# Performance work log

Measured on AMD Instinct MI355X. Metric: run time of the kernel, lower is better.

## Reference

```python
import jax, jax.numpy as jnp
import numpy as np

# cell: per-step concat([x_t, h, cost_t]) -> i2h (Linear to H), i2o (Linear to 1), no bias, no nonlinearity.

P = 16      # prod(kernel) = 4*4
H = 512     # hidden_length
D = P + H + 1  # input_shape = 529


def setup_inputs() -> dict:
    key = jax.random.key(0)
    k1, k2, k3, k4, k5 = jax.random.split(key, 5)
    B, T = 256, 2048
    x = jax.random.normal(k1, (B, T, 4, 4), dtype=jnp.float32)
    hidden = jax.random.normal(k2, (B, H), dtype=jnp.float32)
    cost = jax.random.uniform(k3, (B, T), dtype=jnp.float32)
    # Linear weights (torch convention: [out_features, in_features], bias=False)
    Wo = jax.random.normal(k4, (1, D), dtype=jnp.float32) / np.sqrt(D)
    Wh = jax.random.normal(k5, (H, D), dtype=jnp.float32) / np.sqrt(D)
    return {"x": x, "hidden": hidden, "cost": cost, "Wo": Wo, "Wh": Wh}


def reference(x, hidden, cost, Wo, Wh):
    B, T = x.shape[0], x.shape[1]
    xf = x.reshape(B, T, -1)            # [B, T, P] (flatten(2, -1))
    xs = jnp.swapaxes(xf, 0, 1)         # [T, B, P] for scan over time
    cs = cost.T                         # [T, B]

    def step(h, inp):
        xt, ct = inp                    # xt: [B,P], ct: [B]
        inter = jnp.concatenate([xt, h, ct[:, None]], axis=-1)  # [B, D]
        h_new = inter @ Wh.T            # i2h -> [B, H]
        o = (inter @ Wo.T)[:, 0]        # i2o -> [B], squeeze(-1)
        return h_new, o

    h_final, outs = jax.lax.scan(step, hidden, (xs, cs))
    return outs.T, h_final              # ([B, T], [B, H])
```

## Files before the change

### kernel.cpp

```cpp
#include <hip/hip_runtime.h>


typedef __attribute__((ext_vector_type(8))) _Float16 half8;
typedef __attribute__((ext_vector_type(4))) float f32x4;
typedef unsigned short u16;

#define KTOT 2176
#define NBIG 640

__device__ __forceinline__ u16 f2h(float f) {
  union { _Float16 h; u16 u; } v; v.h = (_Float16)f; return v.u;
}
__device__ __forceinline__ float h2f(u16 u) {
  union { u16 u; _Float16 h; } v; v.u = u; return (float)v.h;
}

typedef const __attribute__((address_space(1))) void* as1cv;
typedef __attribute__((address_space(3))) void* as3v;
__device__ __forceinline__ void gload16(const u16* g, u16* l) {
  __builtin_amdgcn_global_load_lds((as1cv)g, (as3v)l, 16, 0, 0);
}

__device__ __forceinline__ void wave_gemm_acc(const u16* __restrict__ A, int lda,
                                              const u16* __restrict__ Bt, int nstr,
                                              int kc0, int kcN, int lane,
                                              f32x4 (&acc)[4][4]) {
  const int q = lane >> 4, l15 = lane & 15;
  const u16* aP = A + (size_t)l15*lda + (size_t)kc0*32 + q*8;
  const u16* bP = Bt + ((size_t)kc0*nstr + l15)*32 + q*8;
  half8 a[4], b[4];
  #pragma unroll
  for (int rt = 0; rt < 4; ++rt) a[rt] = *(const half8*)(aP + (size_t)(rt*16)*lda);
  #pragma unroll
  for (int ct = 0; ct < 4; ++ct) b[ct] = *(const half8*)(bP + ct*512);
  for (int kc = kc0; kc < kcN; ++kc) {
    const u16* aN = aP + 32;
    const u16* bN = bP + (size_t)nstr*32;
    half8 an[4], bn[4];
    #pragma unroll
    for (int rt = 0; rt < 4; ++rt) an[rt] = *(const half8*)(aN + (size_t)(rt*16)*lda);
    #pragma unroll
    for (int ct = 0; ct < 4; ++ct) bn[ct] = *(const half8*)(bN + ct*512);
    #pragma unroll
    for (int rt = 0; rt < 4; ++rt)
      #pragma unroll
      for (int ct = 0; ct < 4; ++ct)
        acc[rt][ct] = __builtin_amdgcn_mfma_f32_16x16x32_f16(a[rt], b[ct], acc[rt][ct], 0,0,0);
    #pragma unroll
    for (int rt = 0; rt < 4; ++rt) a[rt] = an[rt];
    #pragma unroll
    for (int ct = 0; ct < 4; ++ct) b[ct] = bn[ct];
    aP = aN; bP = bN;
  }
}

__device__ __forceinline__ void wave_gemm(const u16* __restrict__ A, int lda,
                                          const u16* __restrict__ Bt, int nstr,
                                          int kc0, int kcN, int lane,
                                          f32x4 (&acc)[4][4]) {
  #pragma unroll
  for (int rt = 0; rt < 4; ++rt)
    #pragma unroll
    for (int ct = 0; ct < 4; ++ct) { f32x4 z = {0.f,0.f,0.f,0.f}; acc[rt][ct] = z; }
  wave_gemm_acc(A, lda, Bt, nstr, kc0, kcN, lane, acc);
}

__device__ __forceinline__ bool ksplit_reduce(f32x4 (&acc)[4][4], float* red,
                                              int wid, int lane) {
  if (wid > 0) {
    float* dst = red + (wid - 1) * 4096;
    #pragma unroll
    for (int rt = 0; rt < 4; ++rt)
      #pragma unroll
      for (int ct = 0; ct < 4; ++ct)
        *(f32x4*)(dst + ((rt*4 + ct)*64 + lane)*4) = acc[rt][ct];
  }
  __syncthreads();
  if (wid > 0) return false;
  #pragma unroll
  for (int w = 0; w < 3; ++w)
    #pragma unroll
    for (int rt = 0; rt < 4; ++rt)
      #pragma unroll
      for (int ct = 0; ct < 4; ++ct)
        acc[rt][ct] += *(const f32x4*)(red + w*4096 + ((rt*4 + ct)*64 + lane)*4);
  return true;
}

__device__ __forceinline__ void square_tile(const u16* __restrict__ Mp_in,
                                            const u16* __restrict__ Mt_in,
                                            u16* __restrict__ Mp_out,
                                            u16* __restrict__ Mt_out,
                                            int bx, float* red, int tid) {
  const int wid = tid >> 6, lane = tid & 63, q = lane >> 4, l15 = lane & 15;
  int row0 = (bx >> 3) * 64, c0 = (bx & 7) * 64;
  f32x4 acc[4][4];
  wave_gemm(Mp_in + (size_t)row0*512, 512, Mt_in + (size_t)c0*32, 512,
            wid*4, wid*4 + 4, lane, acc);
  if (!ksplit_reduce(acc, red, wid, lane)) return;
  #pragma unroll
  for (int rt = 0; rt < 4; ++rt)
    for (int ct = 0; ct < 4; ++ct)
      for (int r = 0; r < 4; ++r) {
        int row = row0 + rt*16 + q*4 + r, col = c0 + ct*16 + l15;
        u16 v = f2h(acc[rt][ct][r]);
        Mp_out[row*512 + col] = v;
        Mt_out[(row>>5)*16384 + col*32 + (row&31)] = v;
      }
}

__global__ __launch_bounds__(256) void prep_kernel(
    const float* __restrict__ Wh, const float* __restrict__ Wo,
    const float* __restrict__ hidden,
    u16* __restrict__ Mp0, u16* __restrict__ Mt0,
    u16* __restrict__ Sr, float* __restrict__ G,
    float* __restrict__ wod, u16* __restrict__ Hf, u16* __restrict__ Qs) {
  int idx = blockIdx.x * 256 + threadIdx.x;
  if (idx < 262144) {
    int k = idx >> 9, n = idx & 511;
    u16 v = f2h(Wh[n*529 + 16 + k]);
    Mp0[k*512 + n] = v;
    Mt0[(k>>5)*16384 + n*32 + (k&31)] = v;
    return;
  }
  idx -= 262144;
  if (idx < 8704) {
    int q = idx >> 9, n = idx & 511;
    u16 v = f2h(Wh[n*529 + (q < 16 ? q : 528)]);
    Sr[idx] = v;
    Qs[idx] = v;
    return;
  }
  idx -= 8704;
  if (idx < 512) { G[idx*128 + 0] = Wo[16 + idx]; return; }
  idx -= 512;
  if (idx < 17) { wod[idx] = Wo[idx < 16 ? idx : 528]; return; }
  idx -= 17;
  if (idx < 131072) Hf[idx] = f2h(hidden[idx]);
}

__global__ __launch_bounds__(256) void level_kernel(
    const u16* __restrict__ Mp_in, const u16* __restrict__ Mt_in,
    u16* __restrict__ Mp_out, u16* __restrict__ Mt_out,
    u16* __restrict__ Qs, float* __restrict__ G,
    const float* __restrict__ x, const float* __restrict__ cost,
    u16* __restrict__ A, int l) {
  __shared__ float red[12288];
  const int m = 1 << l;
  const int nq8 = (((17*m + 63) >> 6)) * 8;
  const int tid = threadIdx.x, bx = blockIdx.x;
  const int wid = tid >> 6, lane = tid & 63, q = lane >> 4, l15 = lane & 15;

  if (bx < 64) {
    square_tile(Mp_in, Mt_in, Mp_out, Mt_out, bx, red, tid);
    return;
  }
  if (bx < 64 + nq8) {
    int bq = bx - 64;
    int row0 = (bq >> 3) * 64, c0 = (bq & 7) * 64;
    f32x4 acc[4][4];
    wave_gemm(Qs + (size_t)row0*512, 512, Mt_in + (size_t)c0*32, 512,
              wid*4, wid*4 + 4, lane, acc);
    if (!ksplit_reduce(acc, red, wid, lane)) return;
    int lim = 17*m;
    #pragma unroll
    for (int rt = 0; rt < 4; ++rt)
      for (int ct = 0; ct < 4; ++ct)
        for (int r = 0; r < 4; ++r) {
          int rowIn = row0 + rt*16 + q*4 + r, col = c0 + ct*16 + l15;
          if (rowIn < lim) Qs[(size_t)(lim + rowIn)*512 + col] = f2h(acc[rt][ct][r]);
        }
    return;
  }
  if (bx < 64 + nq8 + 32) {
    int n0 = (bx - 64 - nq8) * 16;
    for (int idx = tid; idx < 16*m; idx += 256) {
      int c = idx & (m - 1), n = n0 + (idx >> l);
      const u16* mrow = Mp_in + n*512;
      float s0 = 0.f, s1 = 0.f, s2 = 0.f, s3 = 0.f;
      for (int k = 0; k < 512; k += 4) {
        s0 += h2f(mrow[k])   * G[k*128 + c];
        s1 += h2f(mrow[k+1]) * G[(k+1)*128 + c];
        s2 += h2f(mrow[k+2]) * G[(k+2)*128 + c];
        s3 += h2f(mrow[k+3]) * G[(k+3)*128 + c];
      }
      G[n*128 + m + c] = (s0 + s1) + (s2 + s3);
    }
    return;
  }
  int abx = bx - (64 + nq8 + 32);
  int r = (l*293 + abx)*2 + (tid >> 7);
  if (r >= 4096) return;
  int s = tid & 127;
  int i = r >> 8, b = r & 255, t = i*128 + s;
  const float* xp = x + ((size_t)b*2048 + t)*16;
  u16* ap = A + (size_t)r*KTOT + s*17;
  #pragma unroll
  for (int p = 0; p < 16; p += 4) {
    float4 v = *(const float4*)(xp + p);
    ap[p] = f2h(v.x); ap[p+1] = f2h(v.y); ap[p+2] = f2h(v.z); ap[p+3] = f2h(v.w);
  }
  ap[16] = f2h(cost[(size_t)b*2048 + t]);
}

__global__ void cbar_kernel(const u16* __restrict__ Sr, const float* __restrict__ G,
                            float* __restrict__ Cb) {
  int qq = blockIdx.x, lam = threadIdx.x;
  float s0 = 0.f, s1 = 0.f, s2 = 0.f, s3 = 0.f;
  for (int k = 0; k < 512; k += 4) {
    s0 += h2f(Sr[qq*512 + k])   * G[k*128 + lam];
    s1 += h2f(Sr[qq*512 + k+1]) * G[(k+1)*128 + lam];
    s2 += h2f(Sr[qq*512 + k+2]) * G[(k+2)*128 + lam];
    s3 += h2f(Sr[qq*512 + k+3]) * G[(k+3)*128 + lam];
  }
  Cb[qq*128 + lam] = (s0 + s1) + (s2 + s3);
}

__global__ void bbuild_kernel(const u16* __restrict__ Qs, const float* __restrict__ Cb,
                              const float* __restrict__ wod, const float* __restrict__ G,
                              u16* __restrict__ Bt, u16* __restrict__ Gt) {
  int idx = blockIdx.x * 256 + threadIdx.x;
  if (idx < KTOT * NBIG) {
    int krow = idx / NBIG, n = idx - krow * NBIG;
    int kc = krow >> 5, kk = krow & 31;
    int s = krow / 17, qq = krow - s * 17;
    u16 v;
    if (n < 512) {
      v = Qs[(size_t)((127 - s)*17 + qq)*512 + n];
    } else {
      int j = n - 512;
      if (s < j)       v = f2h(Cb[qq*128 + (j - 1 - s)]);
      else if (s == j) v = f2h(wod[qq]);
      else             v = 0;
    }
    Bt[(size_t)kc*(NBIG*32) + n*32 + kk] = v;
    return;
  }
  idx -= KTOT * NBIG;
  if (idx < 512*128) {
    int k = idx >> 7, j = idx & 127;
    Gt[(k>>5)*4096 + j*32 + (k&31)] = f2h(G[k*128 + j]);
  }
}

__global__ __launch_bounds__(256) void biggemm_kernel(const u16* __restrict__ A,
                                                      const u16* __restrict__ Bt,
                                                      u16* __restrict__ V0,
                                                      float* __restrict__ out,
                                                      const u16* __restrict__ Mp7,
                                                      const u16* __restrict__ Mt7,
                                                      u16* __restrict__ Mp8,
                                                      u16* __restrict__ Mt8) {
  __shared__ __align__(16) char smem[49152];
  const int bx = blockIdx.x, tid = threadIdx.x;
  if (bx >= 160) {
    float* red = (float*)smem;
    square_tile(Mp7, Mt7, Mp8, Mt8, bx - 160, red, tid);
    return;
  }
  u16* sA = (u16*)smem;
  u16* sB = (u16*)(smem + 16384);
  const int rowg = bx & 31, colg = bx >> 5;
  const int row0 = rowg * 128, c0 = colg * 128;
  const int wid = tid >> 6, lane = tid & 63;
  const int q = lane >> 4, l15 = lane & 15;
  const int wr = wid >> 1, wc = wid & 1;
  const int r4 = tid >> 2, ch = tid & 3;

  const u16* gA0 = A + (size_t)(row0 + r4) * KTOT + ch * 8;
  const u16* gB0 = Bt + (size_t)(c0 + r4) * 32 + ch * 8;
  const int lofs = r4 * 32 + ch * 8;

  f32x4 acc[4][4];
  #pragma unroll
  for (int rt = 0; rt < 4; ++rt)
    #pragma unroll
    for (int ct = 0; ct < 4; ++ct) { f32x4 z = {0.f,0.f,0.f,0.f}; acc[rt][ct] = z; }

  gload16(gA0,                     sA + lofs);
  gload16(gA0 + (size_t)64*KTOT,   sA + 2048 + lofs);
  gload16(gB0,                     sB + lofs);
  gload16(gB0 + 64*32,             sB + 2048 + lofs);
  __syncthreads();

  int cur = 0;
  for (int s = 0; s < 68; ++s) {
    if (s + 1 < 68) {
      const u16* ga = gA0 + (s + 1) * 32;
      const u16* gb = gB0 + (size_t)(s + 1) * (NBIG * 32);
      u16* dA = sA + (cur ^ 1) * 4096;
      u16* dB = sB + (cur ^ 1) * 4096;
      gload16(ga,                   dA + lofs);
      gload16(ga + (size_t)64*KTOT, dA + 2048 + lofs);
      gload16(gb,                   dB + lofs);
      gload16(gb + 64*32,           dB + 2048 + lofs);
    }
    const u16* pa = sA + cur * 4096 + (wr*64 + l15) * 32 + q * 8;
    const u16* pb = sB + cur * 4096 + (wc*64 + l15) * 32 + q * 8;
    half8 a[4], b[4];
    #pragma unroll
    for (int rt = 0; rt < 4; ++rt) a[rt] = *(const half8*)(pa + rt*512);
    #pragma unroll
    for (int ct = 0; ct < 4; ++ct) b[ct] = *(const half8*)(pb + ct*512);
    #pragma unroll
    for (int rt = 0; rt < 4; ++rt)
      #pragma unroll
      for (int ct = 0; ct < 4; ++ct)
        acc[rt][ct] = __builtin_amdgcn_mfma_f32_16x16x32_f16(a[rt], b[ct], acc[rt][ct], 0,0,0);
    __syncthreads();
    cur ^= 1;
  }

  #pragma unroll
  for (int rt = 0; rt < 4; ++rt)
    for (int ct = 0; ct < 4; ++ct)
      for (int r = 0; r < 4; ++r) {
        int rg = row0 + wr*64 + rt*16 + q*4 + r;
        int col = c0 + wc*64 + ct*16 + l15;
        if (col < 512) {
          V0[(size_t)rg*512 + col] = f2h(acc[rt][ct][r]);
        } else {
          int j = col - 512, b = rg & 255, i = rg >> 8;
          out[(size_t)b*2048 + i*128 + j] = acc[rt][ct][r];
        }
      }
}

__global__ __launch_bounds__(256) void scan_kernel(const u16* __restrict__ Vsrc,
                                                   u16* __restrict__ Vdst,
                                                   const u16* __restrict__ Mt,
                                                   const u16* __restrict__ Hf, int d,
                                                   int filler,
                                                   const u16* __restrict__ Mp_si,
                                                   const u16* __restrict__ Mt_si,
                                                   u16* __restrict__ Mp_so,
                                                   u16* __restrict__ Mt_so) {
  __shared__ float red[12288];
  const int bx = blockIdx.x, tid = threadIdx.x;
  const int wid = tid >> 6, lane = tid & 63;
  const int q = lane >> 4, l15 = lane & 15;
  if (bx >= 512) {
    if (filler == 1) {
      square_tile(Mp_si, Mt_si, Mp_so, Mt_so, bx - 512, red, tid);
    } else {
      int hbx = bx - 512;
      int rowg = hbx >> 1, colg = hbx & 1;
      int row0 = rowg*64, c0 = colg*64;
      f32x4 acc[4][4];
      wave_gemm(Mp_si + (size_t)row0*512, 512, Mt_si + (size_t)c0*32, 128,
                wid*4, wid*4 + 4, lane, acc);
      if (!ksplit_reduce(acc, red, wid, lane)) return;
      #pragma unroll
      for (int rt = 0; rt < 4; ++rt)
        for (int ct = 0; ct < 4; ++ct)
          for (int r = 0; r < 4; ++r) {
            int n = row0 + rt*16 + q*4 + r, j = c0 + ct*16 + l15;
            Mp_so[(n>>5)*4096 + j*32 + (n&31)] = f2h(acc[rt][ct][r]);
          }
    }
    return;
  }
  int i = bx >> 5, rowg = (bx >> 3) & 3, colg = bx & 7;
  int row0 = rowg*64, c0 = colg*64;
  int src_i = i - d;
  if (src_i >= -1) {
    const u16* Asrc = (src_i >= 0) ? Vsrc + (size_t)(src_i*256 + row0)*512
                                   : Hf + (size_t)row0*512;
    f32x4 acc[4][4];
    wave_gemm(Asrc, 512, Mt + (size_t)c0*32, 512, wid*4, wid*4 + 4, lane, acc);
    if (!ksplit_reduce(acc, red, wid, lane)) return;
    #pragma unroll
    for (int rt = 0; rt < 4; ++rt)
      for (int ct = 0; ct < 4; ++ct)
        for (int r = 0; r < 4; ++r) {
          int rg = i*256 + row0 + rt*16 + q*4 + r, col = c0 + ct*16 + l15;
          Vdst[(size_t)rg*512 + col] = f2h(acc[rt][ct][r] + h2f(Vsrc[(size_t)rg*512 + col]));
        }
  } else {
    for (int it = tid; it < 512; it += 256) {
      int rl = it >> 3, cu = it & 7;
      size_t o = (size_t)(i*256 + row0 + rl)*512 + colg*64 + cu*8;
      *(uint4*)(Vdst + o) = *(const uint4*)(Vsrc + o);
    }
  }
}

__global__ __launch_bounds__(256) void final_kernel(const u16* __restrict__ W,
                                                    const u16* __restrict__ Hf,
                                                    const u16* __restrict__ Gt,
                                                    const u16* __restrict__ G2t,
                                                    const u16* __restrict__ Mt10,
                                                    float* __restrict__ out) {
  __shared__ float red[12288];
  const int bx = blockIdx.x, tid = threadIdx.x;
  const int wid = tid >> 6, lane = tid & 63;
  const int q = lane >> 4, l15 = lane & 15;
  if (bx >= 128) {
    int hbx = bx - 128;
    int rowg = hbx >> 3, colg = hbx & 7;
    int row0 = rowg*64, c0 = colg*64;
    f32x4 acc[4][4];
    wave_gemm(W + (size_t)(1792 + row0)*512, 512, Mt10 + (size_t)c0*32, 512,
              wid*4, wid*4 + 4, lane, acc);
    if (!ksplit_reduce(acc, red, wid, lane)) return;
    #pragma unroll
    for (int rt = 0; rt < 4; ++rt)
      for (int ct = 0; ct < 4; ++ct)
        for (int r = 0; r < 4; ++r) {
          int row = row0 + rt*16 + q*4 + r, col = c0 + ct*16 + l15;
          out[524288 + (size_t)row*512 + col] =
              acc[rt][ct][r] + h2f(W[(size_t)(3840 + row)*512 + col]);
        }
    return;
  }
  int rowg = bx >> 1, colg = bx & 1;
  int row0 = rowg*64, c0 = colg*64;
  int s = rowg >> 2;
  const u16* Abase = (s == 0) ? (Hf + (size_t)row0*512)
                              : (W + (size_t)(row0 - 256)*512);
  f32x4 acc[4][4];
  wave_gemm(Abase, 512, Gt + (size_t)c0*32, 128, wid*4, wid*4 + 4, lane, acc);
  if (s >= 8) {
    int ro = row0 & 255;
    const u16* A2 = (s == 8) ? (Hf + (size_t)ro*512)
                             : (W + (size_t)((s - 9)*256 + ro)*512);
    wave_gemm_acc(A2, 512, G2t + (size_t)c0*32, 128, wid*4, wid*4 + 4, lane, acc);
  }
  if (!ksplit_reduce(acc, red, wid, lane)) return;
  #pragma unroll
  for (int rt = 0; rt < 4; ++rt)
    for (int ct = 0; ct < 4; ++ct)
      for (int r = 0; r < 4; ++r) {
        int rg = row0 + rt*16 + q*4 + r, j = c0 + ct*16 + l15;
        int b = rg & 255, i = rg >> 8;
        out[(size_t)b*2048 + i*128 + j] += acc[rt][ct][r];
      }
}

extern "C" void kernel_launch(void* const* d_in, const int* in_sizes, int n_in,
                              void* d_out, int out_size, void* d_ws, size_t ws_size,
                              hipStream_t stream) {
  (void)in_sizes; (void)n_in; (void)out_size; (void)ws_size;
  const float* x      = (const float*)d_in[0];
  const float* hidden = (const float*)d_in[1];
  const float* cost   = (const float*)d_in[2];
  const float* Wo     = (const float*)d_in[3];
  const float* Wh     = (const float*)d_in[4];
  float* out = (float*)d_out;
  char* ws = (char*)d_ws;

  auto Mp = [&](int l){ return (u16*)(ws + (size_t)l*524288); };
  auto Mt = [&](int l){ return (u16*)(ws + 5767168 + (size_t)l*524288); };
  u16*   Qs  = (u16*)(ws + 11534336);
  float* G   = (float*)(ws + 13762560);
  u16*   Sr  = (u16*)(ws + 14024704);
  float* wod = (float*)(ws + 14057472);
  float* Cb  = (float*)(ws + 14057728);
  u16*   Hf  = (u16*)(ws + 14074112);
  u16*   Bt  = (u16*)(ws + 14336256);
  u16*   Gt  = (u16*)(ws + 17121536);
  u16*   A   = (u16*)(ws + 17252608);
  u16*   V0  = (u16*)(ws + 35078400);
  u16*   V1  = (u16*)(ws + 39272704);
  u16*   G2t = Mp(0);

  prep_kernel<<<1573, 256, 0, stream>>>(Wh, Wo, hidden, Mp(0), Mt(0), Sr, G, wod, Hf, Qs);
  for (int l = 0; l <= 6; ++l) {
    int m = 1 << l;
    int nq8 = ((17*m + 63) >> 6) * 8;
    int abn = (l == 6) ? 290 : 293;
    int grid = 64 + nq8 + 32 + abn;
    level_kernel<<<grid, 256, 0, stream>>>(Mp(l), Mt(l), Mp(l+1), Mt(l+1),
                                           Qs, G, x, cost, A, l);
  }
  cbar_kernel<<<17, 128, 0, stream>>>(Sr, G, Cb);
  bbuild_kernel<<<(KTOT*NBIG + 512*128 + 255)/256, 256, 0, stream>>>(Qs, Cb, wod, G, Bt, Gt);
  biggemm_kernel<<<224, 256, 0, stream>>>(A, Bt, V0, out, Mp(7), Mt(7), Mp(8), Mt(8));
  scan_kernel<<<576, 256, 0, stream>>>(V0, V1, Mt(7), Hf, 1, 1, Mp(8), Mt(8), Mp(9), Mt(9));
  scan_kernel<<<576, 256, 0, stream>>>(V1, V0, Mt(8), Hf, 2, 1, Mp(9), Mt(9), Mp(10), Mt(10));
  scan_kernel<<<528, 256, 0, stream>>>(V0, V1, Mt(9), Hf, 4, 2, Mp(10), Gt, G2t, nullptr);
  final_kernel<<<160, 256, 0, stream>>>(V1, Hf, Gt, G2t, Mt(10), out);
}
```

Measured before the change: 294.6 us.

## Double K-tile depth in big GEMM and XOR-swizzle LDS layout

The big GEMM now stages 64-wide K tiles per pipeline step instead of 32, halving loop iterations and barriers. Shared memory grows to 64KB for the double buffer. The LDS layout uses an XOR swizzle on column chunks by row to reduce bank conflicts on the half8 fragment reads. The larger LDS footprint may lower occupancy, and the square_tile path shares this allocation.

Result: faster. 279.2 us (-5.2%).

```diff
diff --git a/kernel.cpp b/kernel.cpp
--- a/kernel.cpp
+++ b/kernel.cpp
@@ -251,7 +251,7 @@
                                                       const u16* __restrict__ Mt7,
                                                       u16* __restrict__ Mp8,
                                                       u16* __restrict__ Mt8) {
-  __shared__ __align__(16) char smem[49152];
+  __shared__ __align__(16) char smem[65536];
   const int bx = blockIdx.x, tid = threadIdx.x;
   if (bx >= 160) {
     float* red = (float*)smem;
@@ -259,17 +259,17 @@
     return;
   }
   u16* sA = (u16*)smem;
-  u16* sB = (u16*)(smem + 16384);
+  u16* sB = (u16*)(smem + 32768);
   const int rowg = bx & 31, colg = bx >> 5;
   const int row0 = rowg * 128, c0 = colg * 128;
   const int wid = tid >> 6, lane = tid & 63;
   const int q = lane >> 4, l15 = lane & 15;
   const int wr = wid >> 1, wc = wid & 1;
-  const int r4 = tid >> 2, ch = tid & 3;
-
-  const u16* gA0 = A + (size_t)(row0 + r4) * KTOT + ch * 8;
-  const u16* gB0 = Bt + (size_t)(c0 + r4) * 32 + ch * 8;
-  const int lofs = r4 * 32 + ch * 8;
+  const int tr = tid >> 3, tc8 = (tid & 7) * 8;
+  const int swc = tc8 ^ ((tr & 7) << 3);
+  const u16* gA0 = A + (size_t)(row0 + tr) * KTOT + swc;
+  const u16* gB0 = Bt + ((size_t)(swc >> 5) * NBIG + (c0 + tr)) * 32 + (swc & 31);
+  const int lofs = tid * 8;
 
   f32x4 acc[4][4];
   #pragma unroll
@@ -277,36 +277,43 @@
     #pragma unroll
     for (int ct = 0; ct < 4; ++ct) { f32x4 z = {0.f,0.f,0.f,0.f}; acc[rt][ct] = z; }
 
-  gload16(gA0,                     sA + lofs);
-  gload16(gA0 + (size_t)64*KTOT,   sA + 2048 + lofs);
-  gload16(gB0,                     sB + lofs);
-  gload16(gB0 + 64*32,             sB + 2048 + lofs);
+  #pragma unroll
+  for (int j = 0; j < 4; ++j) {
+    gload16(gA0 + (size_t)(32*j)*KTOT, sA + j*2048 + lofs);
+    gload16(gB0 + j*1024,              sB + j*2048 + lofs);
+  }
   __syncthreads();
 
   int cur = 0;
-  for (int s = 0; s < 68; ++s) {
-    if (s + 1 < 68) {
-      const u16* ga = gA0 + (s + 1) * 32;
-      const u16* gb = gB0 + (size_t)(s + 1) * (NBIG * 32);
-      u16* dA = sA + (cur ^ 1) * 4096;
-      u16* dB = sB + (cur ^ 1) * 4096;
-      gload16(ga,                   dA + lofs);
-      gload16(ga + (size_t)64*KTOT, dA + 2048 + lofs);
-      gload16(gb,                   dB + lofs);
-      gload16(gb + 64*32,           dB + 2048 + lofs);
-    }
-    const u16* pa = sA + cur * 4096 + (wr*64 + l15) * 32 + q * 8;
-    const u16* pb = sB + cur * 4096 + (wc*64 + l15) * 32 + q * 8;
-    half8 a[4], b[4];
-    #pragma unroll
-    for (int rt = 0; rt < 4; ++rt) a[rt] = *(const half8*)(pa + rt*512);
-    #pragma unroll
-    for (int ct = 0; ct < 4; ++ct) b[ct] = *(const half8*)(pb + ct*512);
-    #pragma unroll
-    for (int rt = 0; rt < 4; ++rt)
-      #pragma unroll
-      for (int ct = 0; ct < 4; ++ct)
-        acc[rt][ct] = __builtin_amdgcn_mfma_f32_16x16x32_f16(a[rt], b[ct], acc[rt][ct], 0,0,0);
+  for (int s = 0; s < 34; ++s) {
+    if (s + 1 < 34) {
+      const u16* ga = gA0 + (s + 1) * 64;
+      const u16* gb = gB0 + (size_t)(s + 1) * (NBIG * 64);
+      u16* dA = sA + (cur ^ 1) * 8192;
+      u16* dB = sB + (cur ^ 1) * 8192;
+      #pragma unroll
+      for (int j = 0; j < 4; ++j) {
+        gload16(ga + (size_t)(32*j)*KTOT, dA + j*2048 + lofs);
+        gload16(gb + j*1024,              dB + j*2048 + lofs);
+      }
+    }
+    const u16* pA = sA + cur * 8192 + (wr*64 + l15) * 64;
+    const u16* pB = sB + cur * 8192 + (wc*64 + l15) * 64;
+    const int rsw = (l15 & 7) << 3;
+    #pragma unroll
+    for (int kc = 0; kc < 2; ++kc) {
+      const int kcol = (kc*32 + q*8) ^ rsw;
+      half8 a[4], b[4];
+      #pragma unroll
+      for (int rt = 0; rt < 4; ++rt) a[rt] = *(const half8*)(pA + rt*1024 + kcol);
+      #pragma unroll
+      for (int ct = 0; ct < 4; ++ct) b[ct] = *(const half8*)(pB + ct*1024 + kcol);
+      #pragma unroll
+      for (int rt = 0; rt < 4; ++rt)
+        #pragma unroll
+        for (int ct = 0; ct < 4; ++ct)
+          acc[rt][ct] = __builtin_amdgcn_mfma_f32_16x16x32_f16(a[rt], b[ct], acc[rt][ct], 0,0,0);
+    }
     __syncthreads();
     cur ^= 1;
   }
```
